# Optimization experiments

Measured on AMD Instinct MI355X. Metric: run time of the kernel, lower is better.

Reference implementation:

```python
import jax, jax.numpy as jnp
import numpy as np

EMBED_DIM = 1024
NUM_HEADS = 16
HEAD_DIM = EMBED_DIM // NUM_HEADS


def setup_inputs() -> dict:
    key = jax.random.key(0)
    ks = jax.random.split(key, 11)
    B, T, D = 4, 2048, EMBED_DIM
    s = 1.0 / np.sqrt(D)
    inp = {
        "x": jax.random.normal(ks[0], (B, T, D), dtype=jnp.float32),
        "wq": jax.random.normal(ks[1], (D, D), dtype=jnp.float32) * s,
        "bq": jnp.zeros((D,), dtype=jnp.float32),
        "wk": jax.random.normal(ks[2], (D, D), dtype=jnp.float32) * s,
        "bk": jnp.zeros((D,), dtype=jnp.float32),
        "wv": jax.random.normal(ks[3], (D, D), dtype=jnp.float32) * s,
        "bv": jnp.zeros((D,), dtype=jnp.float32),
        "wo": jax.random.normal(ks[4], (D, D), dtype=jnp.float32) * s,
        "bo": jnp.zeros((D,), dtype=jnp.float32),
        "ln_gamma": jnp.ones((D,), dtype=jnp.float32),
        "ln_beta": jnp.zeros((D,), dtype=jnp.float32),
    }
    return inp


def _attention(x, wq, bq, wk, bk, wv, bv, wo, bo, ln_gamma, ln_beta):
    B, T, D = x.shape
    H, Hd = NUM_HEADS, HEAD_DIM
    # projections -> (B, H, T, Hd)
    q = (x @ wq + bq).reshape(B, T, H, Hd).transpose(0, 2, 1, 3)
    k = (x @ wk + bk).reshape(B, T, H, Hd).transpose(0, 2, 1, 3)
    v = (x @ wv + bv).reshape(B, T, H, Hd).transpose(0, 2, 1, 3)
    scores = jnp.einsum("bhqd,bhkd->bhqk", q, k) / jnp.sqrt(jnp.asarray(Hd, x.dtype))
    attn = jax.nn.softmax(scores, axis=-1)  # dropout p=0 -> identity
    out = jnp.einsum("bhqk,bhkd->bhqd", attn, v)
    out = out.transpose(0, 2, 1, 3).reshape(B, T, D)
    out = out @ wo + bo
    # LayerNorm (no residual in the original forward)
    mu = jnp.mean(out, axis=-1, keepdims=True)
    var = jnp.var(out, axis=-1, keepdims=True)
    out = (out - mu) / jnp.sqrt(var + 1e-5) * ln_gamma + ln_beta
    return out


def reference(x, wq, bq, wk, bk, wv, bv, wo, bo, ln_gamma, ln_beta):
    return _attention(x, wq, bq, wk, bk, wv, bv, wo, bo, ln_gamma, ln_beta)
```

## Files before the change

### kernel.cpp

```cpp
#include <hip/hip_runtime.h>
#include <hip/hip_bf16.h>

typedef __bf16 bf16_t;
typedef __bf16 bf16x4v __attribute__((ext_vector_type(4)));
typedef __bf16 bf16x8 __attribute__((ext_vector_type(8)));
typedef float  f32x4  __attribute__((ext_vector_type(4)));

typedef __attribute__((address_space(1))) void* gptr_t;
typedef __attribute__((address_space(3))) void* lptr_t;

#define B_BATCH  4
#define T_SEQ    2048
#define D_MODEL  1024
#define N_HEADS  16
#define HEAD_DIM 64
#define M_ROWS   (B_BATCH * T_SEQ)

#define BM  128
#define BN  128
#define BKK 64
#define LDT 72
#define CPAD 136

#define EXP2_SCALE 0.1803368801111204f

__global__ __launch_bounds__(256) void cvt_x(
    const float* __restrict__ in, bf16_t* __restrict__ out)
{
    const size_t i = ((size_t)blockIdx.x * 256 + threadIdx.x) * 4;
    const f32x4 v = *(const f32x4*)&in[i];
    bf16x4v o;
    for (int e = 0; e < 4; e++) o[e] = (bf16_t)v[e];
    *(bf16x4v*)&out[i] = o;
}

__global__ __launch_bounds__(256) void transpose_w(
    const float* __restrict__ w0, const float* __restrict__ w1,
    const float* __restrict__ w2, const float* __restrict__ w3,
    bf16_t* __restrict__ out)
{
    __shared__ bf16_t tile[32][33];
    const int z = blockIdx.z;
    const float* w = (z == 0) ? w0 : (z == 1) ? w1 : (z == 2) ? w2 : w3;
    bf16_t* o = out + (size_t)z * D_MODEL * D_MODEL;
    const int tx = threadIdx.x & 31, ty = threadIdx.x >> 5;
    const int k0 = blockIdx.y * 32, n0 = blockIdx.x * 32;
    for (int i = 0; i < 4; i++)
        tile[ty + i * 8][tx] = (bf16_t)w[(size_t)(k0 + ty + i * 8) * D_MODEL + n0 + tx];
    __syncthreads();
    for (int i = 0; i < 4; i++)
        o[(size_t)(n0 + ty + i * 8) * D_MODEL + k0 + tx] = tile[tx][ty + i * 8];
}

template <int MODE>
__global__ __launch_bounds__(256) void gemm_k(
    const bf16_t* __restrict__ A, const bf16_t* __restrict__ wT_base,
    const float* __restrict__ b0, const float* __restrict__ b1,
    void* __restrict__ out_base)
{
    __shared__ __attribute__((aligned(16))) bf16_t smem[17408];
    bf16_t (*As)[BKK]  = reinterpret_cast<bf16_t(*)[BKK]>(&smem[0]);
    bf16_t (*Bs)[BKK]  = reinterpret_cast<bf16_t(*)[BKK]>(&smem[8192]);
    bf16_t (*Cs)[CPAD] = reinterpret_cast<bf16_t(*)[CPAD]>(&smem[0]);

    const int tid  = threadIdx.x;
    const int z    = blockIdx.z;
    const bf16_t* BT   = wT_base + (size_t)z * D_MODEL * D_MODEL;
    const float*  bias = (z == 0) ? b0 : b1;
    const int mbase = blockIdx.y * BM;
    const int nbase = blockIdx.x * BN;
    const int w = tid >> 6, lane = tid & 63, quad = lane >> 4, l16 = lane & 15;
    const int wm = (w & 1) * 64, wn = (w >> 1) * 64;
    const int lrow = lane >> 3, lcol = (lane & 7) * 8;

    f32x4 acc[4][4] = {};

    for (int kb = 0; kb < D_MODEL; kb += BKK) {
        __syncthreads();
        for (int it = 0; it < 4; it++) {
            const int r = w * 32 + it * 8;
            __builtin_amdgcn_global_load_lds(
                (gptr_t)&A [(size_t)(mbase + r + lrow) * D_MODEL + kb + lcol],
                (lptr_t)&As[r][0], 16, 0, 0);
            __builtin_amdgcn_global_load_lds(
                (gptr_t)&BT[(size_t)(nbase + r + lrow) * D_MODEL + kb + lcol],
                (lptr_t)&Bs[r][0], 16, 0, 0);
        }
        __syncthreads();
        for (int s = 0; s < 2; s++) {
            bf16x8 af[4], bf[4];
            for (int i = 0; i < 4; i++)
                af[i] = *(const bf16x8*)&As[wm + i * 16 + l16][s * 32 + quad * 8];
            for (int j = 0; j < 4; j++)
                bf[j] = *(const bf16x8*)&Bs[wn + j * 16 + l16][s * 32 + quad * 8];
            for (int i = 0; i < 4; i++)
                for (int j = 0; j < 4; j++)
                    acc[i][j] = __builtin_amdgcn_mfma_f32_16x16x32_bf16(
                        af[i], bf[j], acc[i][j], 0, 0, 0);
        }
    }

    float bj[4];
    for (int j = 0; j < 4; j++)
        bj[j] = bias[nbase + wn + j * 16 + l16];

    if (MODE == 1) {
        for (int i = 0; i < 4; i++)
            for (int r = 0; r < 4; r++) {
                const int rg = mbase + wm + i * 16 + quad * 4 + r;
                for (int j = 0; j < 4; j++) {
                    const int cg = nbase + wn + j * 16 + l16;
                    ((float*)out_base)[(size_t)rg * D_MODEL + cg] = acc[i][j][r] + bj[j];
                }
            }
    } else {
        __syncthreads();
        for (int i = 0; i < 4; i++)
            for (int r = 0; r < 4; r++) {
                const int row = wm + i * 16 + quad * 4 + r;
                for (int j = 0; j < 4; j++) {
                    const int col = wn + j * 16 + l16;
                    const float v = acc[i][j][r] + bj[j];
                    if (MODE == 0) Cs[row][col] = (bf16_t)v;
                    else           Cs[col][row] = (bf16_t)v;
                }
            }
        __syncthreads();

        const int bidx  = mbase >> 11;
        const int t0    = mbase & 2047;
        const int hbase = nbase >> 6;
        bf16_t* outp = (bf16_t*)out_base;
        for (int p = 0; p < 8; p++) {
            const int chunk = p * 256 + tid;
            if (MODE == 0) {
                const int sub = chunk & 7, run = chunk >> 3;
                const int t = run & 127, hl = run >> 7;
                const bf16x8 val = *(const bf16x8*)&Cs[t][hl * 64 + sub * 8];
                bf16_t* q = outp + (size_t)z * ((size_t)M_ROWS * D_MODEL);
                *(bf16x8*)&q[(((size_t)(bidx * N_HEADS + hbase + hl)) * T_SEQ + t0 + t)
                             * HEAD_DIM + sub * 8] = val;
            } else {
                const int sub = chunk & 15, hdl = chunk >> 4;
                const int h = hbase + (hdl >> 6), hd = hdl & 63;
                const bf16x8 val = *(const bf16x8*)&Cs[hdl][sub * 8];
                *(bf16x8*)&outp[(((size_t)(bidx * N_HEADS + h)) * HEAD_DIM + hd) * T_SEQ
                                + t0 + sub * 8] = val;
            }
        }
    }
}

__global__ __launch_bounds__(256, 4) void attn_k(
    const bf16_t* __restrict__ Q, const bf16_t* __restrict__ K,
    const bf16_t* __restrict__ VT, bf16_t* __restrict__ O)
{
    __shared__ __attribute__((aligned(16))) bf16_t Ks[64][LDT];
    __shared__ __attribute__((aligned(16))) bf16_t Vs[64][LDT];
    __shared__ __attribute__((aligned(16))) bf16_t Ps[4][32][LDT];

    const int tid = threadIdx.x;
    const int f = blockIdx.y * 16 + blockIdx.x;
    const int xcd = f & 7, j = f >> 3;
    const int bh = xcd * 8 + (j & 7);
    const int qbase = (j >> 3) * 128;
    const int b = bh >> 4, h = bh & 15;
    const int w = tid >> 6, lane = tid & 63, quad = lane >> 4, l16 = lane & 15;
    const size_t head_off = (size_t)bh * T_SEQ * HEAD_DIM;
    const bf16_t* Qh  = Q  + head_off;
    const bf16_t* Kh  = K  + head_off;
    const bf16_t* VTh = VT + head_off;

    bf16x8 bq[2][2];
    for (int iq = 0; iq < 2; iq++)
        for (int s = 0; s < 2; s++)
            bq[iq][s] = *(const bf16x8*)
                &Qh[(size_t)(qbase + w * 32 + iq * 16 + l16) * HEAD_DIM + s * 32 + quad * 8];

    float l_part[2] = {0.f, 0.f};
    f32x4 Oacc[2][4] = {};

    for (int kt = 0; kt < T_SEQ / 64; kt++) {
        const int kbase = kt * 64;
        __syncthreads();
        for (int it = 0; it < 2; it++) {
            int idx = it * 256 + tid;
            int r = idx >> 3, c8 = (idx & 7) * 8;
            *(bf16x8*)&Ks[r][c8] = *(const bf16x8*)&Kh [(size_t)(kbase + r) * HEAD_DIM + c8];
            *(bf16x8*)&Vs[r][c8] = *(const bf16x8*)&VTh[(size_t)r * T_SEQ + kbase + c8];
        }
        __syncthreads();

        f32x4 St[4][2] = {};
        for (int s = 0; s < 2; s++) {
            bf16x8 ak[4];
            for (int jk = 0; jk < 4; jk++)
                ak[jk] = *(const bf16x8*)&Ks[jk * 16 + l16][s * 32 + quad * 8];
            for (int jk = 0; jk < 4; jk++)
                for (int iq = 0; iq < 2; iq++)
                    St[jk][iq] = __builtin_amdgcn_mfma_f32_16x16x32_bf16(
                        ak[jk], bq[iq][s], St[jk][iq], 0, 0, 0);
        }

        for (int jk = 0; jk < 4; jk++)
            for (int iq = 0; iq < 2; iq++) {
                bf16x4v pv;
                for (int r = 0; r < 4; r++) {
                    const float p = __builtin_amdgcn_exp2f(St[jk][iq][r] * EXP2_SCALE);
                    l_part[iq] += p;
                    pv[r] = (bf16_t)p;
                }
                *(bf16x4v*)&Ps[w][iq * 16 + l16][jk * 16 + quad * 4] = pv;
            }
        asm volatile("" ::: "memory");

        for (int s = 0; s < 2; s++) {
            bf16x8 ap[2], bv[4];
            for (int iq = 0; iq < 2; iq++)
                ap[iq] = *(const bf16x8*)&Ps[w][iq * 16 + l16][s * 32 + quad * 8];
            for (int jn = 0; jn < 4; jn++)
                bv[jn] = *(const bf16x8*)&Vs[jn * 16 + l16][s * 32 + quad * 8];
            for (int iq = 0; iq < 2; iq++)
                for (int jn = 0; jn < 4; jn++)
                    Oacc[iq][jn] = __builtin_amdgcn_mfma_f32_16x16x32_bf16(
                        ap[iq], bv[jn], Oacc[iq][jn], 0, 0, 0);
        }
    }

    for (int iq = 0; iq < 2; iq++) {
        l_part[iq] += __shfl_xor(l_part[iq], 16, 64);
        l_part[iq] += __shfl_xor(l_part[iq], 32, 64);
    }

    for (int iq = 0; iq < 2; iq++) {
        for (int r = 0; r < 4; r++) {
            const int qrow = quad * 4 + r;
            const float inv = 1.f / __shfl(l_part[iq], qrow, 64);
            const int t = qbase + w * 32 + iq * 16 + qrow;
            for (int jn = 0; jn < 4; jn++) {
                const int hd = jn * 16 + l16;
                O[(((size_t)(b * T_SEQ + t)) * N_HEADS + h) * HEAD_DIM + hd] =
                    (bf16_t)(Oacc[iq][jn][r] * inv);
            }
        }
    }
}

__global__ __launch_bounds__(256) void ln_k(
    const float* __restrict__ proj, const float* __restrict__ gamma,
    const float* __restrict__ beta, float* __restrict__ out)
{
    __shared__ float red[4][2];
    const int row = blockIdx.x, tid = threadIdx.x;
    const float* p = proj + (size_t)row * D_MODEL + tid * 4;
    const f32x4 v = *(const f32x4*)p;
    float s1 = v[0] + v[1] + v[2] + v[3];
    float s2 = v[0] * v[0] + v[1] * v[1] + v[2] * v[2] + v[3] * v[3];
    for (int off = 32; off >= 1; off >>= 1) {
        s1 += __shfl_xor(s1, off, 64);
        s2 += __shfl_xor(s2, off, 64);
    }
    const int w = tid >> 6;
    if ((tid & 63) == 0) { red[w][0] = s1; red[w][1] = s2; }
    __syncthreads();
    const float S1 = red[0][0] + red[1][0] + red[2][0] + red[3][0];
    const float S2 = red[0][1] + red[1][1] + red[2][1] + red[3][1];
    const float mu  = S1 * (1.f / D_MODEL);
    const float var = S2 * (1.f / D_MODEL) - mu * mu;
    const float rstd = rsqrtf(var + 1e-5f);
    const int c = tid * 4;
    f32x4 o;
    for (int e = 0; e < 4; e++)
        o[e] = (v[e] - mu) * rstd * gamma[c + e] + beta[c + e];
    *(f32x4*)&out[(size_t)row * D_MODEL + c] = o;
}

extern "C" void kernel_launch(void* const* d_in, const int* in_sizes, int n_in,
                              void* d_out, int out_size, void* d_ws, size_t ws_size,
                              hipStream_t stream)
{
    const float* x  = (const float*)d_in[0];
    const float* wq = (const float*)d_in[1];
    const float* bq = (const float*)d_in[2];
    const float* wk = (const float*)d_in[3];
    const float* bk = (const float*)d_in[4];
    const float* wv = (const float*)d_in[5];
    const float* bv = (const float*)d_in[6];
    const float* wo = (const float*)d_in[7];
    const float* bo = (const float*)d_in[8];
    const float* g  = (const float*)d_in[9];
    const float* be = (const float*)d_in[10];

    char* ws = (char*)d_ws;
    bf16_t* xb   = (bf16_t*)(ws);
    bf16_t* wT   = (bf16_t*)(ws + ((size_t)16 << 20));
    bf16_t* qkv  = (bf16_t*)(ws + ((size_t)24 << 20));
    bf16_t* attn = (bf16_t*)(ws + ((size_t)72 << 20));
    float*  proj = (float*) (ws + ((size_t)88 << 20));
    bf16_t* vt   = (bf16_t*)proj;

    cvt_x<<<dim3(M_ROWS * D_MODEL / 1024), 256, 0, stream>>>(x, xb);
    transpose_w<<<dim3(32, 32, 4), 256, 0, stream>>>(wq, wk, wv, wo, wT);

    gemm_k<0><<<dim3(8, 64, 2), 256, 0, stream>>>(xb, wT, bq, bk, (void*)qkv);
    gemm_k<2><<<dim3(8, 64, 1), 256, 0, stream>>>(
        xb, wT + (size_t)2 * D_MODEL * D_MODEL, bv, bv, (void*)vt);

    bf16_t* Qm = qkv;
    bf16_t* Km = qkv + (size_t)M_ROWS * D_MODEL;

    attn_k<<<dim3(16, 64), 256, 0, stream>>>(Qm, Km, vt, attn);

    gemm_k<1><<<dim3(8, 64, 1), 256, 0, stream>>>(
        attn, wT + (size_t)3 * D_MODEL * D_MODEL, bo, bo, (void*)proj);

    ln_k<<<dim3(M_ROWS), 256, 0, stream>>>(proj, g, be, (float*)d_out);
}
```

Before: 317.0 us.

## Merge QKV GEMM launches, store projection as bf16, pad P tile stride

The Q/K and V GEMMs are merged into one launch with a z dimension of 3, where z selects the bias and the output layout (row-major Q/K or transposed V). The output projection now writes bf16 through a shared-memory staged, coalesced store instead of scattered fp32 stores, and LayerNorm reads bf16. The attention P scratch buffer gets a wider row stride to reduce LDS bank conflicts. These aim to cut a kernel launch, halve the projection write and read traffic, and improve the store pattern. The cost is lower precision in the pre-LayerNorm activations.

Result: slower. 326.2 us (+2.9%).

```diff
diff --git a/kernel.cpp b/kernel.cpp
--- a/kernel.cpp
+++ b/kernel.cpp
@@ -19,7 +19,8 @@
 #define BM  128
 #define BN  128
 #define BKK 64
-#define LDT 72
+#define LDT  72
+#define LDP  80
 #define CPAD 136
 
 #define EXP2_SCALE 0.1803368801111204f
@@ -52,11 +53,11 @@
         o[(size_t)(n0 + ty + i * 8) * D_MODEL + k0 + tx] = tile[tx][ty + i * 8];
 }
 
-template <int MODE>
-__global__ __launch_bounds__(256) void gemm_k(
+__global__ __launch_bounds__(256) void gemm_qkv(
     const bf16_t* __restrict__ A, const bf16_t* __restrict__ wT_base,
     const float* __restrict__ b0, const float* __restrict__ b1,
-    void* __restrict__ out_base)
+    const float* __restrict__ b2, bf16_t* __restrict__ qk_out,
+    bf16_t* __restrict__ vt_out)
 {
     __shared__ __attribute__((aligned(16))) bf16_t smem[17408];
     bf16_t (*As)[BKK]  = reinterpret_cast<bf16_t(*)[BKK]>(&smem[0]);
@@ -66,7 +67,7 @@
     const int tid  = threadIdx.x;
     const int z    = blockIdx.z;
     const bf16_t* BT   = wT_base + (size_t)z * D_MODEL * D_MODEL;
-    const float*  bias = (z == 0) ? b0 : b1;
+    const float*  bias = (z == 0) ? b0 : (z == 1) ? b1 : b2;
     const int mbase = blockIdx.y * BM;
     const int nbase = blockIdx.x * BN;
     const int w = tid >> 6, lane = tid & 63, quad = lane >> 4, l16 = lane & 15;
@@ -104,50 +105,102 @@
     for (int j = 0; j < 4; j++)
         bj[j] = bias[nbase + wn + j * 16 + l16];
 
-    if (MODE == 1) {
-        for (int i = 0; i < 4; i++)
-            for (int r = 0; r < 4; r++) {
-                const int rg = mbase + wm + i * 16 + quad * 4 + r;
-                for (int j = 0; j < 4; j++) {
-                    const int cg = nbase + wn + j * 16 + l16;
-                    ((float*)out_base)[(size_t)rg * D_MODEL + cg] = acc[i][j][r] + bj[j];
-                }
+    __syncthreads();
+    for (int i = 0; i < 4; i++)
+        for (int r = 0; r < 4; r++) {
+            const int row = wm + i * 16 + quad * 4 + r;
+            for (int j = 0; j < 4; j++) {
+                const int col = wn + j * 16 + l16;
+                const float v = acc[i][j][r] + bj[j];
+                if (z != 2) Cs[row][col] = (bf16_t)v;
+                else        Cs[col][row] = (bf16_t)v;
             }
-    } else {
-        __syncthreads();
-        for (int i = 0; i < 4; i++)
-            for (int r = 0; r < 4; r++) {
-                const int row = wm + i * 16 + quad * 4 + r;
-                for (int j = 0; j < 4; j++) {
-                    const int col = wn + j * 16 + l16;
-                    const float v = acc[i][j][r] + bj[j];
-                    if (MODE == 0) Cs[row][col] = (bf16_t)v;
-                    else           Cs[col][row] = (bf16_t)v;
-                }
-            }
-        __syncthreads();
-
-        const int bidx  = mbase >> 11;
-        const int t0    = mbase & 2047;
-        const int hbase = nbase >> 6;
-        bf16_t* outp = (bf16_t*)out_base;
-        for (int p = 0; p < 8; p++) {
-            const int chunk = p * 256 + tid;
-            if (MODE == 0) {
-                const int sub = chunk & 7, run = chunk >> 3;
-                const int t = run & 127, hl = run >> 7;
-                const bf16x8 val = *(const bf16x8*)&Cs[t][hl * 64 + sub * 8];
-                bf16_t* q = outp + (size_t)z * ((size_t)M_ROWS * D_MODEL);
-                *(bf16x8*)&q[(((size_t)(bidx * N_HEADS + hbase + hl)) * T_SEQ + t0 + t)
-                             * HEAD_DIM + sub * 8] = val;
-            } else {
-                const int sub = chunk & 15, hdl = chunk >> 4;
-                const int h = hbase + (hdl >> 6), hd = hdl & 63;
-                const bf16x8 val = *(const bf16x8*)&Cs[hdl][sub * 8];
-                *(bf16x8*)&outp[(((size_t)(bidx * N_HEADS + h)) * HEAD_DIM + hd) * T_SEQ
-                                + t0 + sub * 8] = val;
-            }
-        }
+        }
+    __syncthreads();
+
+    const int bidx  = mbase >> 11;
+    const int t0    = mbase & 2047;
+    const int hbase = nbase >> 6;
+    for (int p = 0; p < 8; p++) {
+        const int chunk = p * 256 + tid;
+        if (z != 2) {
+            const int sub = chunk & 7, run = chunk >> 3;
+            const int t = run & 127, hl = run >> 7;
+            const bf16x8 val = *(const bf16x8*)&Cs[t][hl * 64 + sub * 8];
+            bf16_t* q = qk_out + (size_t)z * ((size_t)M_ROWS * D_MODEL);
+            *(bf16x8*)&q[(((size_t)(bidx * N_HEADS + hbase + hl)) * T_SEQ + t0 + t)
+                         * HEAD_DIM + sub * 8] = val;
+        } else {
+            const int sub = chunk & 15, hdl = chunk >> 4;
+            const int h = hbase + (hdl >> 6), hd = hdl & 63;
+            const bf16x8 val = *(const bf16x8*)&Cs[hdl][sub * 8];
+            *(bf16x8*)&vt_out[(((size_t)(bidx * N_HEADS + h)) * HEAD_DIM + hd) * T_SEQ
+                              + t0 + sub * 8] = val;
+        }
+    }
+}
+
+__global__ __launch_bounds__(256) void gemm_proj(
+    const bf16_t* __restrict__ A, const bf16_t* __restrict__ BT,
+    const float* __restrict__ bias, bf16_t* __restrict__ out)
+{
+    __shared__ __attribute__((aligned(16))) bf16_t smem[17408];
+    bf16_t (*As)[BKK]  = reinterpret_cast<bf16_t(*)[BKK]>(&smem[0]);
+    bf16_t (*Bs)[BKK]  = reinterpret_cast<bf16_t(*)[BKK]>(&smem[8192]);
+    bf16_t (*Cs)[CPAD] = reinterpret_cast<bf16_t(*)[CPAD]>(&smem[0]);
+
+    const int tid  = threadIdx.x;
+    const int mbase = blockIdx.y * BM;
+    const int nbase = blockIdx.x * BN;
+    const int w = tid >> 6, lane = tid & 63, quad = lane >> 4, l16 = lane & 15;
+    const int wm = (w & 1) * 64, wn = (w >> 1) * 64;
+    const int lrow = lane >> 3, lcol = (lane & 7) * 8;
+
+    f32x4 acc[4][4] = {};
+
+    for (int kb = 0; kb < D_MODEL; kb += BKK) {
+        __syncthreads();
+        for (int it = 0; it < 4; it++) {
+            const int r = w * 32 + it * 8;
+            __builtin_amdgcn_global_load_lds(
+                (gptr_t)&A [(size_t)(mbase + r + lrow) * D_MODEL + kb + lcol],
+                (lptr_t)&As[r][0], 16, 0, 0);
+            __builtin_amdgcn_global_load_lds(
+                (gptr_t)&BT[(size_t)(nbase + r + lrow) * D_MODEL + kb + lcol],
+                (lptr_t)&Bs[r][0], 16, 0, 0);
+        }
+        __syncthreads();
+        for (int s = 0; s < 2; s++) {
+            bf16x8 af[4], bf[4];
+            for (int i = 0; i < 4; i++)
+                af[i] = *(const bf16x8*)&As[wm + i * 16 + l16][s * 32 + quad * 8];
+            for (int j = 0; j < 4; j++)
+                bf[j] = *(const bf16x8*)&Bs[wn + j * 16 + l16][s * 32 + quad * 8];
+            for (int i = 0; i < 4; i++)
+                for (int j = 0; j < 4; j++)
+                    acc[i][j] = __builtin_amdgcn_mfma_f32_16x16x32_bf16(
+                        af[i], bf[j], acc[i][j], 0, 0, 0);
+        }
+    }
+
+    float bj[4];
+    for (int j = 0; j < 4; j++)
+        bj[j] = bias[nbase + wn + j * 16 + l16];
+
+    __syncthreads();
+    for (int i = 0; i < 4; i++)
+        for (int r = 0; r < 4; r++) {
+            const int row = wm + i * 16 + quad * 4 + r;
+            for (int j = 0; j < 4; j++)
+                Cs[row][wn + j * 16 + l16] = (bf16_t)(acc[i][j][r] + bj[j]);
+        }
+    __syncthreads();
+
+    for (int p = 0; p < 8; p++) {
+        const int chunk = p * 256 + tid;
+        const int sub = chunk & 15, row = chunk >> 4;
+        const bf16x8 val = *(const bf16x8*)&Cs[row][sub * 8];
+        *(bf16x8*)&out[(size_t)(mbase + row) * D_MODEL + nbase + sub * 8] = val;
     }
 }
 
@@ -157,7 +210,7 @@
 {
     __shared__ __attribute__((aligned(16))) bf16_t Ks[64][LDT];
     __shared__ __attribute__((aligned(16))) bf16_t Vs[64][LDT];
-    __shared__ __attribute__((aligned(16))) bf16_t Ps[4][32][LDT];
+    __shared__ __attribute__((aligned(16))) bf16_t Ps[4][32][LDP];
 
     const int tid = threadIdx.x;
     const int f = blockIdx.y * 16 + blockIdx.x;
@@ -247,13 +300,14 @@
 }
 
 __global__ __launch_bounds__(256) void ln_k(
-    const float* __restrict__ proj, const float* __restrict__ gamma,
+    const bf16_t* __restrict__ proj, const float* __restrict__ gamma,
     const float* __restrict__ beta, float* __restrict__ out)
 {
     __shared__ float red[4][2];
     const int row = blockIdx.x, tid = threadIdx.x;
-    const float* p = proj + (size_t)row * D_MODEL + tid * 4;
-    const f32x4 v = *(const f32x4*)p;
+    const bf16x4v pv = *(const bf16x4v*)&proj[(size_t)row * D_MODEL + tid * 4];
+    f32x4 v;
+    for (int e = 0; e < 4; e++) v[e] = (float)pv[e];
     float s1 = v[0] + v[1] + v[2] + v[3];
     float s2 = v[0] * v[0] + v[1] * v[1] + v[2] * v[2] + v[3] * v[3];
     for (int off = 32; off >= 1; off >>= 1) {
@@ -294,25 +348,23 @@
     char* ws = (char*)d_ws;
     bf16_t* xb   = (bf16_t*)(ws);
     bf16_t* wT   = (bf16_t*)(ws + ((size_t)16 << 20));
-    bf16_t* qkv  = (bf16_t*)(ws + ((size_t)24 << 20));
+    bf16_t* qk   = (bf16_t*)(ws + ((size_t)24 << 20));
     bf16_t* attn = (bf16_t*)(ws + ((size_t)72 << 20));
-    float*  proj = (float*) (ws + ((size_t)88 << 20));
-    bf16_t* vt   = (bf16_t*)proj;
+    bf16_t* vt   = (bf16_t*)(ws + ((size_t)88 << 20));
+    bf16_t* proj = (bf16_t*)(ws + ((size_t)104 << 20));
 
     cvt_x<<<dim3(M_ROWS * D_MODEL / 1024), 256, 0, stream>>>(x, xb);
     transpose_w<<<dim3(32, 32, 4), 256, 0, stream>>>(wq, wk, wv, wo, wT);
 
-    gemm_k<0><<<dim3(8, 64, 2), 256, 0, stream>>>(xb, wT, bq, bk, (void*)qkv);
-    gemm_k<2><<<dim3(8, 64, 1), 256, 0, stream>>>(
-        xb, wT + (size_t)2 * D_MODEL * D_MODEL, bv, bv, (void*)vt);
-
-    bf16_t* Qm = qkv;
-    bf16_t* Km = qkv + (size_t)M_ROWS * D_MODEL;
+    gemm_qkv<<<dim3(8, 64, 3), 256, 0, stream>>>(xb, wT, bq, bk, bv, qk, vt);
+
+    bf16_t* Qm = qk;
+    bf16_t* Km = qk + (size_t)M_ROWS * D_MODEL;
 
     attn_k<<<dim3(16, 64), 256, 0, stream>>>(Qm, Km, vt, attn);
 
-    gemm_k<1><<<dim3(8, 64, 1), 256, 0, stream>>>(
-        attn, wT + (size_t)3 * D_MODEL * D_MODEL, bo, bo, (void*)proj);
+    gemm_proj<<<dim3(8, 64), 256, 0, stream>>>(
+        attn, wT + (size_t)3 * D_MODEL * D_MODEL, bo, proj);
 
     ln_k<<<dim3(M_ROWS), 256, 0, stream>>>(proj, g, be, (float*)d_out);
 }
```
